# Kernel optimization log

Hardware: AMD Instinct MI355X
Metric: run time of the kernel (lower is better)

The kernel has to match this reference:

```python
import jax, jax.numpy as jnp
import numpy as np


def conv2d(x, w, b, pad=0, groups=1):
    y = jax.lax.conv_general_dilated(
        x, w, (1, 1), [(pad, pad), (pad, pad)],
        dimension_numbers=('NCHW', 'OIHW', 'NCHW'), feature_group_count=groups)
    return y + b[None, :, None, None]


def layernorm(x, w, b, eps=1e-5):
    # per-pixel LayerNorm over channel dim (matches to_3d -> nn.LayerNorm(dim) -> to_4d)
    mu = x.mean(1, keepdims=True)
    var = ((x - mu) ** 2).mean(1, keepdims=True)
    return (x - mu) * jax.lax.rsqrt(var + eps) * w[None, :, None, None] + b[None, :, None, None]


def setup_inputs():
    key = jax.random.key(0)
    ks = jax.random.split(key, 16)
    B, C, H, W = 1, 64, 64, 64
    heads, dh = 8, 8
    inner = heads * dh          # 64
    hid_lc = 32                 # max(16, inner // 2)
    hid_f = 4 * C               # 256, ffn_expansion_factor = 4
    def s(k, shape, fan):
        return (jax.random.normal(k, shape, jnp.float32) / np.float32(np.sqrt(fan)))
    return {
        'x': jax.random.normal(ks[0], (B, C, H, W), jnp.float32),
        'luma': jax.random.uniform(ks[1], (B, 1, H, W), jnp.float32),
        'ln1_w': jnp.ones((C,), jnp.float32), 'ln1_b': jnp.zeros((C,), jnp.float32),
        'qkv_w': s(ks[2], (3 * inner, C, 1, 1), C), 'qkv_b': jnp.zeros((3 * inner,), jnp.float32),
        'proj_w': s(ks[3], (C, inner, 1, 1), inner), 'proj_b': jnp.zeros((C,), jnp.float32),
        'lc1_w': s(ks[4], (hid_lc, 1, 3, 3), 9), 'lc1_b': jnp.zeros((hid_lc,), jnp.float32),
        'lc2_w': s(ks[5], (hid_lc, hid_lc, 3, 3), 9 * hid_lc), 'lc2_b': jnp.zeros((hid_lc,), jnp.float32),
        'gam_w': s(ks[6], (inner, hid_lc, 1, 1), hid_lc), 'gam_b': jnp.zeros((inner,), jnp.float32),
        'bet_w': s(ks[7], (inner, hid_lc, 1, 1), hid_lc), 'bet_b': jnp.zeros((inner,), jnp.float32),
        'alpha': jnp.float32(0.1),
        'ln2_w': jnp.ones((C,), jnp.float32), 'ln2_b': jnp.zeros((C,), jnp.float32),
        'ffn1_w': s(ks[8], (hid_f, C, 1, 1), C), 'ffn1_b': jnp.zeros((hid_f,), jnp.float32),
        'dw_w': s(ks[9], (hid_f, 1, 3, 3), 9), 'dw_b': jnp.zeros((hid_f,), jnp.float32),
        'ffn2_w': s(ks[10], (C, hid_f, 1, 1), hid_f), 'ffn2_b': jnp.zeros((C,), jnp.float32),
    }


def reference(x, luma, ln1_w, ln1_b, qkv_w, qkv_b, proj_w, proj_b,
              lc1_w, lc1_b, lc2_w, lc2_b, gam_w, gam_b, bet_w, bet_b, alpha,
              ln2_w, ln2_b, ffn1_w, ffn1_b, dw_w, dw_b, ffn2_w, ffn2_b):
    B, C, H, W = x.shape
    heads = 8
    N = H * W
    # --- attention branch ---
    xn = layernorm(x, ln1_w, ln1_b)
    qkv = conv2d(xn, qkv_w, qkv_b)             # [B, 3*inner, H, W]
    inner = qkv.shape[1] // 3
    dh = inner // heads

    def to_bhnd(t):  # b (h d) x y -> b h (x y) d
        return t.reshape(B, heads, dh, N).transpose(0, 1, 3, 2)

    q, k, v = [to_bhnd(t) for t in jnp.split(qkv, 3, axis=1)]
    # luma conditioning
    h1 = jax.nn.relu(conv2d(luma, lc1_w, lc1_b, pad=1))
    h1 = jax.nn.relu(conv2d(h1, lc2_w, lc2_b, pad=1))
    g = to_bhnd(conv2d(h1, gam_w, gam_b))
    bt = to_bhnd(conv2d(h1, bet_w, bet_b))
    q = g * q + bt
    k = g * k + bt
    v = g * v + bt
    # additive luma bias on q (avg_pool2d 3x3, count_include_pad=True -> fixed /9)
    invL = 1.0 - luma
    invL = jax.lax.reduce_window(invL, 0.0, jax.lax.add, (1, 1, 3, 3), (1, 1, 1, 1),
                                 [(0, 0), (0, 0), (1, 1), (1, 1)]) / 9.0
    invL = invL.reshape(B, N)
    invL = invL - invL.mean(-1, keepdims=True)
    q = q + alpha * invL[:, None, :, None]
    scale = dh ** -0.5
    attn = jax.nn.softmax(jnp.einsum('bhid,bhjd->bhij', q, k) * scale, axis=-1)
    out = jnp.einsum('bhij,bhjd->bhid', attn, v)
    out = out.transpose(0, 1, 3, 2).reshape(B, inner, H, W)
    x = x + conv2d(out, proj_w, proj_b)
    # --- ConvFFN branch ---
    y = layernorm(x, ln2_w, ln2_b)
    y = conv2d(y, ffn1_w, ffn1_b)
    y = conv2d(y, dw_w, dw_b, pad=1, groups=y.shape[1])
    y = jax.nn.gelu(y, approximate=False)
    y = conv2d(y, ffn2_w, ffn2_b)
    return x + y
```

## Files before the change

kernel.cpp:

```cpp
#include <hip/hip_runtime.h>
#include <math.h>

#define NPIX 4096
#define IMG 64

typedef __attribute__((ext_vector_type(8))) short bf16x8;
typedef __attribute__((ext_vector_type(4))) float floatx4;
typedef __attribute__((ext_vector_type(4))) unsigned int uintx4;

__device__ __forceinline__ unsigned int split_pack(float x) {
  unsigned int u = __float_as_uint(x);
  unsigned int hif = u & 0xffff0000u;
  float lof = x - __uint_as_float(hif);
  return (u >> 16) | (__float_as_uint(lof) & 0xffff0000u);
}

__device__ __forceinline__ unsigned int hi_pair(float a, float b) {
  return (__float_as_uint(a) >> 16) | (__float_as_uint(b) & 0xffff0000u);
}

__global__ __launch_bounds__(256) void lc1_kernel(
    const float* __restrict__ luma, const float* __restrict__ w1,
    const float* __restrict__ b1, float* __restrict__ h1,
    float* __restrict__ pooled, float* __restrict__ bsums,
    unsigned short* __restrict__ cbuf) {
  __shared__ float red[256];
  int tile = blockIdx.x, ocg = blockIdx.y;
  int tid = threadIdx.x;
  if (tile == 0 && ocg == 0 && tid < 16) cbuf[tid] = (tid < 8) ? 0x3F80 : 0;
  int p = tile * 256 + tid;
  int py = p >> 6, px = p & 63;
  float v[9];
#pragma unroll
  for (int dy = 0; dy < 3; dy++)
#pragma unroll
    for (int dx = 0; dx < 3; dx++) {
      int y = py + dy - 1, x = px + dx - 1;
      v[dy * 3 + dx] =
          (y >= 0 && y < IMG && x >= 0 && x < IMG) ? luma[y * IMG + x] : 0.f;
    }
#pragma unroll
  for (int o = 0; o < 4; o++) {
    int oc = ocg * 4 + o;
    float s = b1[oc];
#pragma unroll
    for (int t = 0; t < 9; t++) s = fmaf(w1[oc * 9 + t], v[t], s);
    h1[oc * NPIX + p] = fmaxf(s, 0.f);
  }
  if (ocg == 0) {
    float sv = 0.f;
#pragma unroll
    for (int t = 0; t < 9; t++) sv += v[t];
    float cy = 3.f - (py == 0 ? 1.f : 0.f) - (py == 63 ? 1.f : 0.f);
    float cx = 3.f - (px == 0 ? 1.f : 0.f) - (px == 63 ? 1.f : 0.f);
    float pv = (cy * cx - sv) * (1.f / 9.f);
    pooled[p] = pv;
    red[tid] = pv;
    __syncthreads();
    for (int st = 128; st > 0; st >>= 1) {
      if (tid < st) red[tid] += red[tid + st];
      __syncthreads();
    }
    if (tid == 0) bsums[tile] = red[0];
  }
}

__global__ __launch_bounds__(256) void lc2_kernel(
    const float* __restrict__ h1, const float* __restrict__ w2,
    const float* __restrict__ b2, const float* __restrict__ x,
    float* __restrict__ h2, float* __restrict__ mu1, float* __restrict__ rs1) {
  __shared__ float tin[32][324];
  __shared__ float swt[4][32][9];
  int tile = blockIdx.x, ocg = blockIdx.y;
  int ty0 = (tile >> 2) * 16, tx0 = (tile & 3) * 16;
  int tid = threadIdx.x;
  for (int idx = tid; idx < 32 * 324; idx += 256) {
    int ic = idx / 324, pos = idx - ic * 324;
    int py = pos / 18, px = pos - py * 18;
    int gy = ty0 + py - 1, gx = tx0 + px - 1;
    tin[ic][pos] = (gy >= 0 && gy < IMG && gx >= 0 && gx < IMG)
                       ? h1[ic * NPIX + gy * IMG + gx]
                       : 0.f;
  }
  for (int idx = tid; idx < 4 * 32 * 9; idx += 256) {
    int o = idx / 288, r = idx - o * 288;
    swt[o][r / 9][r % 9] = w2[(ocg * 4 + o) * 288 + r];
  }
  __syncthreads();
  int ly = tid >> 4, lx = tid & 15;
  int p = (ty0 + ly) * IMG + tx0 + lx;
  float acc[4];
#pragma unroll
  for (int o = 0; o < 4; o++) acc[o] = b2[ocg * 4 + o];
  for (int ic = 0; ic < 32; ic++) {
    float v[9];
#pragma unroll
    for (int dy = 0; dy < 3; dy++)
#pragma unroll
      for (int dx = 0; dx < 3; dx++)
        v[dy * 3 + dx] = tin[ic][(ly + dy) * 18 + lx + dx];
#pragma unroll
    for (int o = 0; o < 4; o++)
#pragma unroll
      for (int t = 0; t < 9; t++) acc[o] = fmaf(swt[o][ic][t], v[t], acc[o]);
  }
#pragma unroll
  for (int o = 0; o < 4; o++)
    h2[(ocg * 4 + o) * NPIX + p] = fmaxf(acc[o], 0.f);
  if (ocg == 0) {
    float s = 0.f, q = 0.f;
#pragma unroll 8
    for (int cc = 0; cc < 64; cc++) {
      float xv = x[cc * NPIX + p];
      s += xv;
      q = fmaf(xv, xv, q);
    }
    float mu = s * (1.f / 64.f);
    mu1[p] = mu;
    rs1[p] = rsqrtf(q * (1.f / 64.f) - mu * mu + 1e-5f);
  }
}

__global__ __launch_bounds__(256) void ln_qkv_kernel(
    const float* __restrict__ X, const float* __restrict__ mu1,
    const float* __restrict__ rs1, const float* __restrict__ lnw,
    const float* __restrict__ lnb, const float* __restrict__ W,
    const float* __restrict__ bias, const float* __restrict__ gamW,
    const float* __restrict__ gamB, const float* __restrict__ betW,
    const float* __restrict__ betB, const float* __restrict__ h2,
    const float* __restrict__ pooled, const float* __restrict__ bsums,
    const float* __restrict__ alpha, unsigned short* __restrict__ qhl,
    unsigned short* __restrict__ khl, unsigned short* __restrict__ vthx,
    unsigned short* __restrict__ vtlx) {
  const float QSCALE = 0.35355339059327376f * 1.4426950408889634f;
  __shared__ float xs[64][32];
  __shared__ float wsh[64][64];
  __shared__ float h2s[32][32];
  __shared__ float wgs[32][64];
  __shared__ float wbs[32][64];
  __shared__ float mu[32];
  __shared__ float rs[32];
  int n0 = blockIdx.x * 32, part = blockIdx.y, m0 = part * 64;
  int tid = threadIdx.x;
  if (tid < 32) {
    mu[tid] = mu1[n0 + tid];
    rs[tid] = rs1[n0 + tid];
  }
  {
    int e = tid * 2;
    int c = e >> 3, off = (e & 7) * 4;
    *(float4*)&xs[c][off] = *(const float4*)&X[c * NPIX + n0 + off];
    int e1 = e + 1;
    int c1 = e1 >> 3, off1 = (e1 & 7) * 4;
    *(float4*)&xs[c1][off1] = *(const float4*)&X[c1 * NPIX + n0 + off1];
  }
  {
    int m = tid >> 2, kg = (tid & 3) * 16;
    const float4* wr = (const float4*)&W[(m0 + m) * 64 + kg];
    float4 w0 = wr[0], w1 = wr[1], w2 = wr[2], w3 = wr[3];
    float wv[16] = {w0.x, w0.y, w0.z, w0.w, w1.x, w1.y, w1.z, w1.w,
                    w2.x, w2.y, w2.z, w2.w, w3.x, w3.y, w3.z, w3.w};
#pragma unroll
    for (int j = 0; j < 16; j++) wsh[kg + j][m] = wv[j];
  }
  {
    int k = tid >> 3, nf = (tid & 7) * 4;
    *(float4*)&h2s[k][nf] = *(const float4*)&h2[k * NPIX + n0 + nf];
  }
  {
    int m = tid >> 2, kg = (tid & 3) * 8;
    const float4* g0 = (const float4*)&gamW[m * 32 + kg];
    float4 a = g0[0], b4 = g0[1];
    float gv[8] = {a.x, a.y, a.z, a.w, b4.x, b4.y, b4.z, b4.w};
#pragma unroll
    for (int j = 0; j < 8; j++) wgs[kg + j][m] = gv[j];
    const float4* bb0 = (const float4*)&betW[m * 32 + kg];
    float4 c4 = bb0[0], d4 = bb0[1];
    float bv[8] = {c4.x, c4.y, c4.z, c4.w, d4.x, d4.y, d4.z, d4.w};
#pragma unroll
    for (int j = 0; j < 8; j++) wbs[kg + j][m] = bv[j];
  }
  __syncthreads();
  {
    int c = tid >> 2, pg = (tid & 3) * 8;
    float wc = lnw[c], bc = lnb[c];
#pragma unroll
    for (int j = 0; j < 8; j++) {
      int p = pg + j;
      xs[c][p] = (xs[c][p] - mu[p]) * rs[p] * wc + bc;
    }
  }
  __syncthreads();
  int tx = tid & 15, ty = tid >> 4;
  float ga[4][2] = {}, ba[4][2] = {};
#pragma unroll 8
  for (int kk = 0; kk < 32; kk++) {
    float4 wg4 = *(const float4*)&wgs[kk][ty * 4];
    float4 wb4 = *(const float4*)&wbs[kk][ty * 4];
    float2 h22 = *(const float2*)&h2s[kk][tx * 2];
    float gv[4] = {wg4.x, wg4.y, wg4.z, wg4.w};
    float bv[4] = {wb4.x, wb4.y, wb4.z, wb4.w};
    float hv[2] = {h22.x, h22.y};
#pragma unroll
    for (int im = 0; im < 4; im++)
#pragma unroll
      for (int in = 0; in < 2; in++) {
        ga[im][in] = fmaf(gv[im], hv[in], ga[im][in]);
        ba[im][in] = fmaf(bv[im], hv[in], ba[im][in]);
      }
  }
#pragma unroll
  for (int im = 0; im < 4; im++) {
    int cc = ty * 4 + im;
    float gb = gamB[cc], bb2 = betB[cc];
#pragma unroll
    for (int in = 0; in < 2; in++) {
      ga[im][in] += gb;
      ba[im][in] += bb2;
    }
  }
  float acc[4][2] = {};
#pragma unroll 8
  for (int kk = 0; kk < 64; kk++) {
    float4 a = *(const float4*)&wsh[kk][ty * 4];
    float2 b2 = *(const float2*)&xs[kk][tx * 2];
    float av[4] = {a.x, a.y, a.z, a.w};
    float bv[2] = {b2.x, b2.y};
#pragma unroll
    for (int im = 0; im < 4; im++)
#pragma unroll
      for (int in = 0; in < 2; in++)
        acc[im][in] = fmaf(av[im], bv[in], acc[im][in]);
  }
  float val[4][2];
#pragma unroll
  for (int im = 0; im < 4; im++) {
    int cc = ty * 4 + im;
    float bv = bias[m0 + cc];
#pragma unroll
    for (int in = 0; in < 2; in++)
      val[im][in] = fmaf(ga[im][in], acc[im][in] + bv, ba[im][in]);
  }
  if (part == 0) {
    float msum = 0.f;
#pragma unroll
    for (int t = 0; t < 16; t++) msum += bsums[t];
    float mean = msum * (1.f / 4096.f);
    float a0 = alpha[0];
    const float2 pv = *(const float2*)&pooled[n0 + tx * 2];
    float iv[2] = {a0 * (pv.x - mean), a0 * (pv.y - mean)};
#pragma unroll
    for (int im = 0; im < 4; im++)
#pragma unroll
      for (int in = 0; in < 2; in++)
        val[im][in] = (val[im][in] + iv[in]) * QSCALE;
  }
  if (part < 2) {
    unsigned short* dst = (part == 0) ? qhl : khl;
    int h = ty >> 1, d0 = (ty & 1) * 4;
#pragma unroll
    for (int in = 0; in < 2; in++) {
      int n = n0 + tx * 2 + in;
      unsigned int pk[4];
#pragma unroll
      for (int im = 0; im < 4; im++) pk[im] = split_pack(val[im][in]);
      short4 hi, lo;
      hi.x = (short)(pk[0] & 0xffffu); hi.y = (short)(pk[1] & 0xffffu);
      hi.z = (short)(pk[2] & 0xffffu); hi.w = (short)(pk[3] & 0xffffu);
      lo.x = (short)(pk[0] >> 16); lo.y = (short)(pk[1] >> 16);
      lo.z = (short)(pk[2] >> 16); lo.w = (short)(pk[3] >> 16);
      unsigned short* base = dst + ((size_t)(h * NPIX + n) << 4) + d0;
      *(short4*)base = hi;
      *(short4*)(base + 8) = lo;
    }
  } else {
    int nq = n0 + tx * 2;
    int off0 = (nq >> 5) * 32 + ((nq >> 4) & 1) * 4 + ((nq >> 2) & 3) * 8 +
               (nq & 3);
#pragma unroll
    for (int im = 0; im < 4; im++) {
      int cc = ty * 4 + im;
      unsigned int pk0 = split_pack(val[im][0]);
      unsigned int pk1 = split_pack(val[im][1]);
      short2 hi, lo;
      hi.x = (short)(pk0 & 0xffffu);
      hi.y = (short)(pk1 & 0xffffu);
      lo.x = (short)(pk0 >> 16);
      lo.y = (short)(pk1 >> 16);
      *(short2*)(vthx + (size_t)cc * NPIX + off0) = hi;
      *(short2*)(vtlx + (size_t)cc * NPIX + off0) = lo;
    }
  }
}

__global__ __launch_bounds__(256, 4) void attn_kernel(
    const unsigned short* __restrict__ qhl,
    const unsigned short* __restrict__ khl,
    const unsigned short* __restrict__ vthx,
    const unsigned short* __restrict__ vtlx,
    const unsigned short* __restrict__ cbuf, float* __restrict__ pacc,
    float* __restrict__ pl) {
  int tid = threadIdx.x;
  int wave = tid >> 6, lane = tid & 63;
  int g = lane >> 4, c = lane & 15;
  int h = blockIdx.y, jp = blockIdx.z;
  int i0 = blockIdx.x * 256 + wave * 64;
  int jbase = jp * 512;
  bf16x8 qB[4];
#pragma unroll
  for (int t = 0; t < 4; t++)
    qB[t] = *(const bf16x8*)(qhl + ((size_t)(h * NPIX + i0 + t * 16 + c) << 4) +
                             ((g & 1) << 3));
  const unsigned short* kp =
      khl + ((size_t)(h * NPIX + jbase + c) << 4) + ((g >> 1) << 3);
  const unsigned short* vhp;
  const unsigned short* vlp;
  int vstep;
  if (c < 8) {
    vhp = vthx + (size_t)(h * 8 + c) * NPIX + jbase + (g << 3);
    vlp = vtlx + (size_t)(h * 8 + c) * NPIX + jbase + (g << 3);
    vstep = 32;
  } else {
    vhp = (c == 8) ? cbuf : (cbuf + 8);
    vlp = cbuf + 8;
    vstep = 0;
  }
  floatx4 zero4 = {0.f, 0.f, 0.f, 0.f};
  floatx4 aH[4], aM[4];
#pragma unroll
  for (int t = 0; t < 4; t++) {
    aH[t] = zero4;
    aM[t] = zero4;
  }
#pragma unroll 2
  for (int jt = 0; jt < 16; ++jt) {
    bf16x8 ka0 = *(const bf16x8*)kp;
    bf16x8 ka1 = *(const bf16x8*)(kp + 256);
    bf16x8 avh = *(const bf16x8*)vhp;
    bf16x8 avl = *(const bf16x8*)vlp;
    kp += 512;
    vhp += vstep;
    vlp += vstep;
#pragma unroll
    for (int t = 0; t < 4; t++) {
      floatx4 s0 =
          __builtin_amdgcn_mfma_f32_16x16x32_bf16(ka0, qB[t], zero4, 0, 0, 0);
      floatx4 s1 =
          __builtin_amdgcn_mfma_f32_16x16x32_bf16(ka1, qB[t], zero4, 0, 0, 0);
      float p0 = __builtin_amdgcn_exp2f(fminf(s0[0], 80.f));
      float p1 = __builtin_amdgcn_exp2f(fminf(s0[1], 80.f));
      float p2 = __builtin_amdgcn_exp2f(fminf(s0[2], 80.f));
      float p3 = __builtin_amdgcn_exp2f(fminf(s0[3], 80.f));
      float p4 = __builtin_amdgcn_exp2f(fminf(s1[0], 80.f));
      float p5 = __builtin_amdgcn_exp2f(fminf(s1[1], 80.f));
      float p6 = __builtin_amdgcn_exp2f(fminf(s1[2], 80.f));
      float p7 = __builtin_amdgcn_exp2f(fminf(s1[3], 80.f));
      uintx4 bh;
      bh.x = hi_pair(p0, p1);
      bh.y = hi_pair(p2, p3);
      bh.z = hi_pair(p4, p5);
      bh.w = hi_pair(p6, p7);
      bf16x8 pbh = __builtin_bit_cast(bf16x8, bh);
      aH[t] = __builtin_amdgcn_mfma_f32_16x16x32_bf16(avh, pbh, aH[t], 0, 0, 0);
      aM[t] = __builtin_amdgcn_mfma_f32_16x16x32_bf16(avl, pbh, aM[t], 0, 0, 0);
    }
  }
#pragma unroll
  for (int t = 0; t < 4; t++) {
    floatx4 o = aH[t] + aM[t];
    if (g < 2) {
      size_t b0 = (size_t)((jp * 8 + h) * NPIX + i0 + t * 16 + c);
      *(float4*)&pacc[b0 * 8 + g * 4] = make_float4(o[0], o[1], o[2], o[3]);
    } else if (g == 2) {
      pl[(size_t)((jp * 8 + h) * NPIX + i0 + t * 16 + c)] = o[0];
    }
  }
}

__global__ __launch_bounds__(256) void proj_ffn1_kernel(
    const float* __restrict__ pacc, const float* __restrict__ pl,
    const float* __restrict__ Wp, const float* __restrict__ bp,
    const float* __restrict__ x, const float* __restrict__ ln2w,
    const float* __restrict__ ln2b, const float* __restrict__ W1,
    const float* __restrict__ b1f, float* __restrict__ x1,
    float* __restrict__ f1) {
  __shared__ float at[64][33];
  __shared__ float wsh[64][64];
  __shared__ float xsl[64][33];
  __shared__ float ps[8][33];
  __shared__ float pq[8][33];
  __shared__ float mus[32];
  __shared__ float rss[32];
  int n0 = blockIdx.x * 32;
  int ch = blockIdx.y;
  int tid = threadIdx.x;
  {
    int mm = tid >> 2, kg = (tid & 3) * 16;
    const float4* wr = (const float4*)&Wp[mm * 64 + kg];
    float4 w0 = wr[0], w1 = wr[1], w2 = wr[2], w3 = wr[3];
    float wv[16] = {w0.x, w0.y, w0.z, w0.w, w1.x, w1.y, w1.z, w1.w,
                    w2.x, w2.y, w2.z, w2.w, w3.x, w3.y, w3.z, w3.w};
#pragma unroll
    for (int j = 0; j < 16; j++) wsh[kg + j][mm] = wv[j];
  }
  {
    int hh = tid >> 5, nn = tid & 31;
    int i = n0 + nn;
    float L = 0.f, o[8] = {};
#pragma unroll
    for (int p = 0; p < 8; p++) {
      size_t base = (size_t)((p * 8 + hh) * NPIX + i);
      L += pl[base];
      const float4 a0 = *(const float4*)&pacc[base * 8];
      const float4 a1 = *(const float4*)&pacc[base * 8 + 4];
      o[0] += a0.x; o[1] += a0.y; o[2] += a0.z; o[3] += a0.w;
      o[4] += a1.x; o[5] += a1.y; o[6] += a1.z; o[7] += a1.w;
    }
    float inv = 1.f / L;
#pragma unroll
    for (int d = 0; d < 8; d++) at[hh * 8 + d][nn] = o[d] * inv;
  }
  __syncthreads();
  int ty = tid >> 5, tx = tid & 31;
  float acc[8] = {};
#pragma unroll 8
  for (int k = 0; k < 64; k++) {
    float b = at[k][tx];
    float4 a0 = *(const float4*)&wsh[k][ty * 8];
    float4 a1 = *(const float4*)&wsh[k][ty * 8 + 4];
    acc[0] = fmaf(a0.x, b, acc[0]);
    acc[1] = fmaf(a0.y, b, acc[1]);
    acc[2] = fmaf(a0.z, b, acc[2]);
    acc[3] = fmaf(a0.w, b, acc[3]);
    acc[4] = fmaf(a1.x, b, acc[4]);
    acc[5] = fmaf(a1.y, b, acc[5]);
    acc[6] = fmaf(a1.z, b, acc[6]);
    acc[7] = fmaf(a1.w, b, acc[7]);
  }
  float v[8], sn = 0.f, qn = 0.f;
#pragma unroll
  for (int im = 0; im < 8; im++) {
    int row = ty * 8 + im;
    float vv = acc[im] + bp[row] + x[row * NPIX + n0 + tx];
    v[im] = vv;
    sn += vv;
    qn = fmaf(vv, vv, qn);
  }
  if (ch == 0) {
#pragma unroll
    for (int im = 0; im < 8; im++)
      x1[(ty * 8 + im) * NPIX + n0 + tx] = v[im];
  }
  ps[ty][tx] = sn;
  pq[ty][tx] = qn;
  __syncthreads();
  if (tid < 32) {
    float s = 0.f, q = 0.f;
#pragma unroll
    for (int t = 0; t < 8; t++) {
      s += ps[t][tid];
      q += pq[t][tid];
    }
    float mu = s * (1.f / 64.f);
    mus[tid] = mu;
    rss[tid] = rsqrtf(q * (1.f / 64.f) - mu * mu + 1e-5f);
  }
  __syncthreads();
  {
    float muv = mus[tx], rsv = rss[tx];
#pragma unroll
    for (int im = 0; im < 8; im++) {
      int row = ty * 8 + im;
      xsl[row][tx] = (v[im] - muv) * rsv * ln2w[row] + ln2b[row];
    }
  }
  {
    int mm = tid >> 2, kg = (tid & 3) * 16;
    const float4* wr = (const float4*)&W1[(ch * 64 + mm) * 64 + kg];
    float4 w0 = wr[0], w1 = wr[1], w2 = wr[2], w3 = wr[3];
    float wv[16] = {w0.x, w0.y, w0.z, w0.w, w1.x, w1.y, w1.z, w1.w,
                    w2.x, w2.y, w2.z, w2.w, w3.x, w3.y, w3.z, w3.w};
#pragma unroll
    for (int j = 0; j < 16; j++) wsh[kg + j][mm] = wv[j];
  }
  __syncthreads();
  float a2[8] = {};
#pragma unroll 8
  for (int k = 0; k < 64; k++) {
    float b = xsl[k][tx];
    float4 a0 = *(const float4*)&wsh[k][ty * 8];
    float4 a1 = *(const float4*)&wsh[k][ty * 8 + 4];
    a2[0] = fmaf(a0.x, b, a2[0]);
    a2[1] = fmaf(a0.y, b, a2[1]);
    a2[2] = fmaf(a0.z, b, a2[2]);
    a2[3] = fmaf(a0.w, b, a2[3]);
    a2[4] = fmaf(a1.x, b, a2[4]);
    a2[5] = fmaf(a1.y, b, a2[5]);
    a2[6] = fmaf(a1.z, b, a2[6]);
    a2[7] = fmaf(a1.w, b, a2[7]);
  }
#pragma unroll
  for (int im = 0; im < 8; im++) {
    int row = ch * 64 + ty * 8 + im;
    f1[row * NPIX + n0 + tx] = a2[im] + b1f[row];
  }
}

__global__ __launch_bounds__(256) void dw_gelu_kernel(
    const float* __restrict__ f1, const float* __restrict__ w,
    const float* __restrict__ b, float* __restrict__ f2) {
  int t = blockIdx.x * 256 + threadIdx.x;
  int c = t >> 10, pq = t & 1023;
  int py = pq >> 4, px0 = (pq & 15) << 2;
  const float* base = f1 + c * NPIX;
  float wv[9];
#pragma unroll
  for (int i = 0; i < 9; i++) wv[i] = w[c * 9 + i];
  float bc = b[c];
  float a[4] = {bc, bc, bc, bc};
#pragma unroll
  for (int dy = 0; dy < 3; dy++) {
    int y = py + dy - 1;
    if (y < 0 || y > 63) continue;
    const float* row = base + y * IMG + px0;
    float4 mid = *(const float4*)row;
    float left = (px0 > 0) ? row[-1] : 0.f;
    float right = (px0 < 60) ? row[4] : 0.f;
    float win[6] = {left, mid.x, mid.y, mid.z, mid.w, right};
#pragma unroll
    for (int o = 0; o < 4; o++)
#pragma unroll
      for (int dx = 0; dx < 3; dx++)
        a[o] = fmaf(wv[dy * 3 + dx], win[o + dx], a[o]);
  }
  float4 o4;
  float* op = &o4.x;
#pragma unroll
  for (int o = 0; o < 4; o++)
    op[o] = 0.5f * a[o] * (1.f + erff(a[o] * 0.70710678118654752f));
  *(float4*)&f2[c * NPIX + py * IMG + px0] = o4;
}

__global__ __launch_bounds__(256) void ffn2_kernel(
    const float* __restrict__ W, const float* __restrict__ X,
    const float* __restrict__ bias, const float* __restrict__ resid,
    float* __restrict__ C) {
  __shared__ float xs[256][32];
  __shared__ float wsh[256][16];
  int n0 = blockIdx.x * 32, m0 = blockIdx.y * 16;
  int tid = threadIdx.x;
#pragma unroll
  for (int e = tid; e < 2048; e += 256) {
    int k = e >> 3, nf = (e & 7) * 4;
    *(float4*)&xs[k][nf] = *(const float4*)&X[k * NPIX + n0 + nf];
  }
#pragma unroll
  for (int e = tid; e < 4096; e += 256) {
    int mm = e >> 8, kk = e & 255;
    wsh[kk][mm] = W[(m0 + mm) * 256 + kk];
  }
  __syncthreads();
  int m = tid >> 4, np = (tid & 15) * 2;
  float acc0 = 0.f, acc1 = 0.f;
#pragma unroll 8
  for (int kk = 0; kk < 256; kk++) {
    float a = wsh[kk][m];
    float2 b2 = *(const float2*)&xs[kk][np];
    acc0 = fmaf(a, b2.x, acc0);
    acc1 = fmaf(a, b2.y, acc1);
  }
  int row = m0 + m;
  float bv = bias[row];
  const float2 r2 = *(const float2*)&resid[row * NPIX + n0 + np];
  float2 o = make_float2(acc0 + bv + r2.x, acc1 + bv + r2.y);
  *(float2*)&C[row * NPIX + n0 + np] = o;
}

extern "C" void kernel_launch(void* const* d_in, const int* in_sizes, int n_in,
                              void* d_out, int out_size, void* d_ws,
                              size_t ws_size, hipStream_t stream) {
  const float* x      = (const float*)d_in[0];
  const float* luma   = (const float*)d_in[1];
  const float* ln1_w  = (const float*)d_in[2];
  const float* ln1_b  = (const float*)d_in[3];
  const float* qkv_w  = (const float*)d_in[4];
  const float* qkv_b  = (const float*)d_in[5];
  const float* proj_w = (const float*)d_in[6];
  const float* proj_b = (const float*)d_in[7];
  const float* lc1_w  = (const float*)d_in[8];
  const float* lc1_b  = (const float*)d_in[9];
  const float* lc2_w  = (const float*)d_in[10];
  const float* lc2_b  = (const float*)d_in[11];
  const float* gam_w  = (const float*)d_in[12];
  const float* gam_b  = (const float*)d_in[13];
  const float* bet_w  = (const float*)d_in[14];
  const float* bet_b  = (const float*)d_in[15];
  const float* alpha  = (const float*)d_in[16];
  const float* ln2_w  = (const float*)d_in[17];
  const float* ln2_b  = (const float*)d_in[18];
  const float* ffn1_w = (const float*)d_in[19];
  const float* ffn1_b = (const float*)d_in[20];
  const float* dw_w   = (const float*)d_in[21];
  const float* dw_b   = (const float*)d_in[22];
  const float* ffn2_w = (const float*)d_in[23];
  const float* ffn2_b = (const float*)d_in[24];
  float* out = (float*)d_out;

  float* w = (float*)d_ws;
  float* pooled = w + 0;
  float* bsums  = w + 4096;
  unsigned short* cbuf = (unsigned short*)(w + 4160);
  float* mu1 = w + 4224;
  float* rs1 = w + 8320;
  unsigned short* qhl  = (unsigned short*)(w + 12416);
  unsigned short* khl  = (unsigned short*)(w + 274560);
  unsigned short* vthx = (unsigned short*)(w + 536704);
  unsigned short* vtlx = (unsigned short*)(w + 667776);
  float* pacc = w + 798848;
  float* pl   = w + 2896000;
  float* x1   = w + 3158144;
  float* f1   = w + 3420288;
  float* f2   = w + 4468864;
  float* h2   = w + 5517440;
  float* h1   = w + 5648512;

  lc1_kernel<<<dim3(16, 8), 256, 0, stream>>>(luma, lc1_w, lc1_b, h1, pooled,
                                              bsums, cbuf);
  lc2_kernel<<<dim3(16, 8), 256, 0, stream>>>(h1, lc2_w, lc2_b, x, h2, mu1,
                                              rs1);
  ln_qkv_kernel<<<dim3(128, 3), 256, 0, stream>>>(
      x, mu1, rs1, ln1_w, ln1_b, qkv_w, qkv_b, gam_w, gam_b, bet_w, bet_b, h2,
      pooled, bsums, alpha, qhl, khl, vthx, vtlx);
  attn_kernel<<<dim3(16, 8, 8), 256, 0, stream>>>(qhl, khl, vthx, vtlx, cbuf,
                                                  pacc, pl);
  proj_ffn1_kernel<<<dim3(128, 4), 256, 0, stream>>>(
      pacc, pl, proj_w, proj_b, x, ln2_w, ln2_b, ffn1_w, ffn1_b, x1, f1);
  dw_gelu_kernel<<<1024, 256, 0, stream>>>(f1, dw_w, dw_b, f2);
  ffn2_kernel<<<dim3(128, 4), 256, 0, stream>>>(ffn2_w, f2, ffn2_b, x1, out);
}
```

Baseline: 202.5 us.

## Fuse luma conv stages and depthwise-GELU into ffn2 GEMM

Merges the two luma-conditioning convolutions into one kernel that recomputes the first conv's ReLU output directly into shared memory from a padded luma tile, so the h1 buffer is never written to or read from global memory. It also folds the depthwise 3x3 conv and GELU into the ffn2 kernel, which builds its input tile in shared memory instead of reading a precomputed f2 buffer, and widens the output tile to 32 rows with a 2x2 register block per thread. This removes two launches and two global round trips. In exchange the ffn2 grid drops to 256 blocks, each block has more shared memory and work, and the depthwise work is redone for every M tile (twice).

```diff
diff --git a/kernel.cpp b/kernel.cpp
--- a/kernel.cpp
+++ b/kernel.cpp
@@ -19,40 +19,83 @@
   return (__float_as_uint(a) >> 16) | (__float_as_uint(b) & 0xffff0000u);
 }
 
-__global__ __launch_bounds__(256) void lc1_kernel(
+__global__ __launch_bounds__(256) void lc12_kernel(
     const float* __restrict__ luma, const float* __restrict__ w1,
-    const float* __restrict__ b1, float* __restrict__ h1,
-    float* __restrict__ pooled, float* __restrict__ bsums,
-    unsigned short* __restrict__ cbuf) {
+    const float* __restrict__ b1, const float* __restrict__ w2,
+    const float* __restrict__ b2, const float* __restrict__ x,
+    float* __restrict__ h2, float* __restrict__ pooled,
+    float* __restrict__ bsums, float* __restrict__ mu1,
+    float* __restrict__ rs1, unsigned short* __restrict__ cbuf) {
+  __shared__ float lum[400];
+  __shared__ float sw1[288];
+  __shared__ float tin[32][324];
+  __shared__ float swt[4][32][9];
   __shared__ float red[256];
   int tile = blockIdx.x, ocg = blockIdx.y;
+  int ty0 = (tile >> 2) * 16, tx0 = (tile & 3) * 16;
   int tid = threadIdx.x;
   if (tile == 0 && ocg == 0 && tid < 16) cbuf[tid] = (tid < 8) ? 0x3F80 : 0;
-  int p = tile * 256 + tid;
-  int py = p >> 6, px = p & 63;
-  float v[9];
-#pragma unroll
-  for (int dy = 0; dy < 3; dy++)
-#pragma unroll
-    for (int dx = 0; dx < 3; dx++) {
-      int y = py + dy - 1, x = px + dx - 1;
-      v[dy * 3 + dx] =
-          (y >= 0 && y < IMG && x >= 0 && x < IMG) ? luma[y * IMG + x] : 0.f;
-    }
-#pragma unroll
-  for (int o = 0; o < 4; o++) {
-    int oc = ocg * 4 + o;
-    float s = b1[oc];
-#pragma unroll
-    for (int t = 0; t < 9; t++) s = fmaf(w1[oc * 9 + t], v[t], s);
-    h1[oc * NPIX + p] = fmaxf(s, 0.f);
-  }
+  for (int idx = tid; idx < 400; idx += 256) {
+    int py = idx / 20, px = idx - py * 20;
+    int gy = ty0 + py - 2, gx = tx0 + px - 2;
+    lum[idx] = (gy >= 0 && gy < IMG && gx >= 0 && gx < IMG)
+                   ? luma[gy * IMG + gx]
+                   : 0.f;
+  }
+  for (int idx = tid; idx < 288; idx += 256) sw1[idx] = w1[idx];
+  for (int idx = tid; idx < 1152; idx += 256) {
+    int o = idx / 288, r = idx - o * 288;
+    swt[o][r / 9][r % 9] = w2[(ocg * 4 + o) * 288 + r];
+  }
+  __syncthreads();
+  for (int idx = tid; idx < 32 * 324; idx += 256) {
+    int ic = idx / 324, pos = idx - ic * 324;
+    int py = pos / 18, px = pos - py * 18;
+    int gy = ty0 + py - 1, gx = tx0 + px - 1;
+    float v = 0.f;
+    if (gy >= 0 && gy < IMG && gx >= 0 && gx < IMG) {
+      float s = b1[ic];
+      const float* wp = &sw1[ic * 9];
+#pragma unroll
+      for (int dy = 0; dy < 3; dy++)
+#pragma unroll
+        for (int dx = 0; dx < 3; dx++)
+          s = fmaf(wp[dy * 3 + dx], lum[(py + dy) * 20 + px + dx], s);
+      v = fmaxf(s, 0.f);
+    }
+    tin[ic][pos] = v;
+  }
+  __syncthreads();
+  int ly = tid >> 4, lx = tid & 15;
+  int p = (ty0 + ly) * IMG + tx0 + lx;
+  float acc[4];
+#pragma unroll
+  for (int o = 0; o < 4; o++) acc[o] = b2[ocg * 4 + o];
+  for (int ic = 0; ic < 32; ic++) {
+    float v[9];
+#pragma unroll
+    for (int dy = 0; dy < 3; dy++)
+#pragma unroll
+      for (int dx = 0; dx < 3; dx++)
+        v[dy * 3 + dx] = tin[ic][(ly + dy) * 18 + lx + dx];
+#pragma unroll
+    for (int o = 0; o < 4; o++)
+#pragma unroll
+      for (int t = 0; t < 9; t++) acc[o] = fmaf(swt[o][ic][t], v[t], acc[o]);
+  }
+#pragma unroll
+  for (int o = 0; o < 4; o++)
+    h2[(ocg * 4 + o) * NPIX + p] = fmaxf(acc[o], 0.f);
   if (ocg == 0) {
+    int gy = ty0 + ly, gx = tx0 + lx;
     float sv = 0.f;
 #pragma unroll
-    for (int t = 0; t < 9; t++) sv += v[t];
-    float cy = 3.f - (py == 0 ? 1.f : 0.f) - (py == 63 ? 1.f : 0.f);
-    float cx = 3.f - (px == 0 ? 1.f : 0.f) - (px == 63 ? 1.f : 0.f);
+    for (int dy = 0; dy < 3; dy++)
+#pragma unroll
+      for (int dx = 0; dx < 3; dx++)
+        sv += lum[(ly + dy + 1) * 20 + lx + dx + 1];
+    float cy = 3.f - (gy == 0 ? 1.f : 0.f) - (gy == 63 ? 1.f : 0.f);
+    float cx = 3.f - (gx == 0 ? 1.f : 0.f) - (gx == 63 ? 1.f : 0.f);
     float pv = (cy * cx - sv) * (1.f / 9.f);
     pooled[p] = pv;
     red[tid] = pv;
@@ -62,52 +105,6 @@
       __syncthreads();
     }
     if (tid == 0) bsums[tile] = red[0];
-  }
-}
-
-__global__ __launch_bounds__(256) void lc2_kernel(
-    const float* __restrict__ h1, const float* __restrict__ w2,
-    const float* __restrict__ b2, const float* __restrict__ x,
-    float* __restrict__ h2, float* __restrict__ mu1, float* __restrict__ rs1) {
-  __shared__ float tin[32][324];
-  __shared__ float swt[4][32][9];
-  int tile = blockIdx.x, ocg = blockIdx.y;
-  int ty0 = (tile >> 2) * 16, tx0 = (tile & 3) * 16;
-  int tid = threadIdx.x;
-  for (int idx = tid; idx < 32 * 324; idx += 256) {
-    int ic = idx / 324, pos = idx - ic * 324;
-    int py = pos / 18, px = pos - py * 18;
-    int gy = ty0 + py - 1, gx = tx0 + px - 1;
-    tin[ic][pos] = (gy >= 0 && gy < IMG && gx >= 0 && gx < IMG)
-                       ? h1[ic * NPIX + gy * IMG + gx]
-                       : 0.f;
-  }
-  for (int idx = tid; idx < 4 * 32 * 9; idx += 256) {
-    int o = idx / 288, r = idx - o * 288;
-    swt[o][r / 9][r % 9] = w2[(ocg * 4 + o) * 288 + r];
-  }
-  __syncthreads();
-  int ly = tid >> 4, lx = tid & 15;
-  int p = (ty0 + ly) * IMG + tx0 + lx;
-  float acc[4];
-#pragma unroll
-  for (int o = 0; o < 4; o++) acc[o] = b2[ocg * 4 + o];
-  for (int ic = 0; ic < 32; ic++) {
-    float v[9];
-#pragma unroll
-    for (int dy = 0; dy < 3; dy++)
-#pragma unroll
-      for (int dx = 0; dx < 3; dx++)
-        v[dy * 3 + dx] = tin[ic][(ly + dy) * 18 + lx + dx];
-#pragma unroll
-    for (int o = 0; o < 4; o++)
-#pragma unroll
-      for (int t = 0; t < 9; t++) acc[o] = fmaf(swt[o][ic][t], v[t], acc[o]);
-  }
-#pragma unroll
-  for (int o = 0; o < 4; o++)
-    h2[(ocg * 4 + o) * NPIX + p] = fmaxf(acc[o], 0.f);
-  if (ocg == 0) {
     float s = 0.f, q = 0.f;
 #pragma unroll 8
     for (int cc = 0; cc < 64; cc++) {
@@ -506,74 +503,78 @@
   }
 }
 
-__global__ __launch_bounds__(256) void dw_gelu_kernel(
-    const float* __restrict__ f1, const float* __restrict__ w,
-    const float* __restrict__ b, float* __restrict__ f2) {
-  int t = blockIdx.x * 256 + threadIdx.x;
-  int c = t >> 10, pq = t & 1023;
-  int py = pq >> 4, px0 = (pq & 15) << 2;
-  const float* base = f1 + c * NPIX;
-  float wv[9];
-#pragma unroll
-  for (int i = 0; i < 9; i++) wv[i] = w[c * 9 + i];
-  float bc = b[c];
-  float a[4] = {bc, bc, bc, bc};
-#pragma unroll
-  for (int dy = 0; dy < 3; dy++) {
-    int y = py + dy - 1;
-    if (y < 0 || y > 63) continue;
-    const float* row = base + y * IMG + px0;
-    float4 mid = *(const float4*)row;
-    float left = (px0 > 0) ? row[-1] : 0.f;
-    float right = (px0 < 60) ? row[4] : 0.f;
-    float win[6] = {left, mid.x, mid.y, mid.z, mid.w, right};
-#pragma unroll
-    for (int o = 0; o < 4; o++)
-#pragma unroll
-      for (int dx = 0; dx < 3; dx++)
-        a[o] = fmaf(wv[dy * 3 + dx], win[o + dx], a[o]);
-  }
-  float4 o4;
-  float* op = &o4.x;
-#pragma unroll
-  for (int o = 0; o < 4; o++)
-    op[o] = 0.5f * a[o] * (1.f + erff(a[o] * 0.70710678118654752f));
-  *(float4*)&f2[c * NPIX + py * IMG + px0] = o4;
-}
-
-__global__ __launch_bounds__(256) void ffn2_kernel(
-    const float* __restrict__ W, const float* __restrict__ X,
+__global__ __launch_bounds__(256) void ffn2_dw_kernel(
+    const float* __restrict__ f1, const float* __restrict__ dww,
+    const float* __restrict__ dwb, const float* __restrict__ W,
     const float* __restrict__ bias, const float* __restrict__ resid,
     float* __restrict__ C) {
-  __shared__ float xs[256][32];
-  __shared__ float wsh[256][16];
-  int n0 = blockIdx.x * 32, m0 = blockIdx.y * 16;
+  __shared__ float xs[256][36];
+  __shared__ float wsh[256][33];
+  int n0 = blockIdx.x * 32, m0 = blockIdx.y * 32;
   int tid = threadIdx.x;
-#pragma unroll
-  for (int e = tid; e < 2048; e += 256) {
-    int k = e >> 3, nf = (e & 7) * 4;
-    *(float4*)&xs[k][nf] = *(const float4*)&X[k * NPIX + n0 + nf];
-  }
-#pragma unroll
-  for (int e = tid; e < 4096; e += 256) {
+  int y = n0 >> 6, x0 = n0 & 63;
+#pragma unroll
+  for (int e = tid; e < 8192; e += 256) {
     int mm = e >> 8, kk = e & 255;
     wsh[kk][mm] = W[(m0 + mm) * 256 + kk];
   }
-  __syncthreads();
-  int m = tid >> 4, np = (tid & 15) * 2;
-  float acc0 = 0.f, acc1 = 0.f;
+  {
+    int px4 = (tid & 7) * 4;
+    int xabs = x0 + px4;
+#pragma unroll
+    for (int k = 0; k < 8; k++) {
+      int c = (tid >> 3) + 32 * k;
+      const float* base = f1 + c * NPIX;
+      float wv[9];
+#pragma unroll
+      for (int i = 0; i < 9; i++) wv[i] = dww[c * 9 + i];
+      float bc = dwb[c];
+      float a[4] = {bc, bc, bc, bc};
+#pragma unroll
+      for (int dy = 0; dy < 3; dy++) {
+        int yy = y + dy - 1;
+        if (yy < 0 || yy > 63) continue;
+        const float* row = base + yy * IMG + xabs;
+        float4 mid = *(const float4*)row;
+        float left = (xabs > 0) ? row[-1] : 0.f;
+        float right = (xabs + 4 < IMG) ? row[4] : 0.f;
+        float win[6] = {left, mid.x, mid.y, mid.z, mid.w, right};
+#pragma unroll
+        for (int o = 0; o < 4; o++)
+#pragma unroll
+          for (int dx = 0; dx < 3; dx++)
+            a[o] = fmaf(wv[dy * 3 + dx], win[o + dx], a[o]);
+      }
+      float4 o4;
+      float* op = &o4.x;
+#pragma unroll
+      for (int o = 0; o < 4; o++)
+        op[o] = 0.5f * a[o] * (1.f + erff(a[o] * 0.70710678118654752f));
+      *(float4*)&xs[c][px4] = o4;
+    }
+  }
+  __syncthreads();
+  int m2 = (tid >> 4) * 2, np = (tid & 15) * 2;
+  float a00 = 0.f, a01 = 0.f, a10 = 0.f, a11 = 0.f;
 #pragma unroll 8
   for (int kk = 0; kk < 256; kk++) {
-    float a = wsh[kk][m];
-    float2 b2 = *(const float2*)&xs[kk][np];
-    acc0 = fmaf(a, b2.x, acc0);
-    acc1 = fmaf(a, b2.y, acc1);
-  }
-  int row = m0 + m;
-  float bv = bias[row];
-  const float2 r2 = *(const float2*)&resid[row * NPIX + n0 + np];
-  float2 o = make_float2(acc0 + bv + r2.x, acc1 + bv + r2.y);
-  *(float2*)&C[row * NPIX + n0 + np] = o;
+    float w0 = wsh[kk][m2];
+    float w1 = wsh[kk][m2 + 1];
+    float b0 = xs[kk][np];
+    float b1 = xs[kk][np + 1];
+    a00 = fmaf(w0, b0, a00);
+    a01 = fmaf(w0, b1, a01);
+    a10 = fmaf(w1, b0, a10);
+    a11 = fmaf(w1, b1, a11);
+  }
+  int r0 = m0 + m2, r1 = r0 + 1;
+  float bv0 = bias[r0], bv1 = bias[r1];
+  const float2 rr0 = *(const float2*)&resid[r0 * NPIX + n0 + np];
+  const float2 rr1 = *(const float2*)&resid[r1 * NPIX + n0 + np];
+  *(float2*)&C[r0 * NPIX + n0 + np] =
+      make_float2(a00 + bv0 + rr0.x, a01 + bv0 + rr0.y);
+  *(float2*)&C[r1 * NPIX + n0 + np] =
+      make_float2(a10 + bv1 + rr1.x, a11 + bv1 + rr1.y);
 }
 
 extern "C" void kernel_launch(void* const* d_in, const int* in_sizes, int n_in,
@@ -620,14 +621,11 @@
   float* pl   = w + 2896000;
   float* x1   = w + 3158144;
   float* f1   = w + 3420288;
-  float* f2   = w + 4468864;
-  float* h2   = w + 5517440;
-  float* h1   = w + 5648512;
-
-  lc1_kernel<<<dim3(16, 8), 256, 0, stream>>>(luma, lc1_w, lc1_b, h1, pooled,
-                                              bsums, cbuf);
-  lc2_kernel<<<dim3(16, 8), 256, 0, stream>>>(h1, lc2_w, lc2_b, x, h2, mu1,
-                                              rs1);
+  float* h2   = w + 4468864;
+
+  lc12_kernel<<<dim3(16, 8), 256, 0, stream>>>(luma, lc1_w, lc1_b, lc2_w,
+                                               lc2_b, x, h2, pooled, bsums,
+                                               mu1, rs1, cbuf);
   ln_qkv_kernel<<<dim3(128, 3), 256, 0, stream>>>(
       x, mu1, rs1, ln1_w, ln1_b, qkv_w, qkv_b, gam_w, gam_b, bet_w, bet_b, h2,
       pooled, bsums, alpha, qhl, khl, vthx, vtlx);
@@ -635,6 +633,6 @@
                                                   pacc, pl);
   proj_ffn1_kernel<<<dim3(128, 4), 256, 0, stream>>>(
       pacc, pl, proj_w, proj_b, x, ln2_w, ln2_b, ffn1_w, ffn1_b, x1, f1);
-  dw_gelu_kernel<<<1024, 256, 0, stream>>>(f1, dw_w, dw_b, f2);
-  ffn2_kernel<<<dim3(128, 4), 256, 0, stream>>>(ffn2_w, f2, ffn2_b, x1, out);
-}
+  ffn2_dw_kernel<<<dim3(128, 2), 256, 0, stream>>>(f1, dw_w, dw_b, ffn2_w,
+                                                   ffn2_b, x1, out);
+}
```

Result: faster. 195.9 us (-3.3%).
